# Kernel tuning notes

Measured on AMD Instinct MI355X. Metric: run time of the kernel, lower is better.

Reference implementation:

```python
import jax, jax.numpy as jnp
import numpy as np

# WAGE-style quantizer (NeuroSim training path): round to 2^(b-1) levels, clip to (-1+1/S, 1-1/S),
# straight-through estimator for gradients.

def wage_q(x, bits=8):
    S = 2.0 ** (bits - 1)
    q = jnp.clip(jnp.round(x * S) / S, -1.0 + 1.0 / S, 1.0 - 1.0 / S)
    return x + jax.lax.stop_gradient(q - x)


def qconv(x, w, stride, pad, wl_w=8, wl_a=8):
    wq = wage_q(w, wl_w)
    y = jax.lax.conv_general_dilated(
        x, wq, window_strides=(stride, stride),
        padding=[(pad, pad), (pad, pad)],
        dimension_numbers=('NCHW', 'OIHW', 'NCHW'))
    return wage_q(y, wl_a)


def pad_hw(x, p):
    return jnp.pad(x, ((0, 0), (0, 0), (p, p), (p, p)))


def crop_like(x, tgt):
    return x[:, :, :tgt.shape[2], :tgt.shape[3]]


WEIGHT_SHAPES = {
    'w1': (64, 4, 3, 3), 'w2': (128, 64, 3, 3), 'w3': (256, 128, 3, 3), 'w4': (512, 256, 3, 3),
    'wr11': (512, 512, 3, 3), 'wr12': (512, 512, 3, 3), 'wr21': (512, 512, 3, 3), 'wr22': (512, 512, 3, 3),
    'wd3': (128, 512, 4, 4), 'wd2': (64, 416, 4, 4), 'wd1': (4, 224, 4, 4),
    'wu43': (32, 512, 4, 4), 'wu32': (32, 416, 4, 4), 'wu21': (32, 224, 4, 4), 'wu10': (32, 100, 4, 4),
    'wfc': (1, 32),
}


def setup_inputs() -> dict:
    key = jax.random.key(0)
    keys = jax.random.split(key, len(WEIGHT_SHAPES) + 1)
    inp = {'x': jax.random.normal(keys[0], (8, 4, 256, 256), dtype=jnp.float32)}
    for i, (name, shp) in enumerate(WEIGHT_SHAPES.items()):
        fan_in = int(np.prod(shp[1:]))
        inp[name] = jax.random.normal(keys[i + 1], shp, dtype=jnp.float32) / np.sqrt(fan_in)
    return inp


def reference(x, w1, w2, w3, w4, wr11, wr12, wr21, wr22,
              wd3, wd2, wd1, wu43, wu32, wu21, wu10, wfc):
    c1 = qconv(x, w1, 2, 1)        # [B,64,128,128]
    c2 = qconv(c1, w2, 2, 1)       # [B,128,64,64]
    c3 = qconv(c2, w3, 2, 1)       # [B,256,32,32]
    c4 = qconv(c3, w4, 2, 1)       # [B,512,16,16]
    r11 = qconv(c4, wr11, 1, 1)
    r12 = (1.0 - qconv(r11, wr12, 1, 1)) * c4
    r21 = qconv(r12, wr21, 1, 1)
    r22 = (1.0 - qconv(r21, wr22, 1, 1)) * r12
    r22p = pad_hw(r22, 8)                                   # [B,512,32,32]
    flow4_up = crop_like(qconv(r22p, wu43, 1, 2), c3)       # [B,32,32,32]
    d3 = crop_like(qconv(r22p, wd3, 1, 2), c3)              # [B,128,32,32]
    cat3 = pad_hw(jnp.concatenate([c3, d3, flow4_up], 1), 16)  # [B,416,64,64]
    flow3_up = crop_like(qconv(cat3, wu32, 1, 2), c2)
    d2 = crop_like(qconv(cat3, wd2, 1, 2), c2)
    cat2 = pad_hw(jnp.concatenate([c2, d2, flow3_up], 1), 32)  # [B,224,128,128]
    flow2_up = crop_like(qconv(cat2, wu21, 1, 2), c1)
    d1 = crop_like(qconv(cat2, wd1, 1, 2), c1)
    cat1 = pad_hw(jnp.concatenate([c1, d1, flow2_up], 1), 64)  # [B,100,256,256]
    u10 = qconv(cat1, wu10, 1, 2)                              # [B,32,257,257]
    feat = jnp.max(u10, axis=(2, 3))                           # AdaptiveMaxPool2d((1,1))
    out = wage_q(feat @ wage_q(wfc, 8).T, 8)                   # QLinear 32->1
    return out
```

## Files before the change

### kernel.cpp

```cpp
#include <hip/hip_runtime.h>

#define DEV __device__ __forceinline__

typedef __attribute__((ext_vector_type(4))) int i32x4;

DEV int wqi(float y) {
    int q = (int)rintf(y * 128.0f);
    return q < -127 ? -127 : (q > 127 ? 127 : q);
}
DEV unsigned encf(float f) { unsigned u = __float_as_uint(f); return (u & 0x80000000u) ? ~u : (u | 0x80000000u); }
DEV float decf(unsigned u) { return (u & 0x80000000u) ? __uint_as_float(u ^ 0x80000000u) : __uint_as_float(~u); }
DEV float wq8f(float x) {
    float q = rintf(x * 128.0f) * 0.0078125f;
    return fminf(fmaxf(q, -0.9921875f), 0.9921875f);
}

#define GLOAD16(g, l) __builtin_amdgcn_global_load_lds( \
    (const __attribute__((address_space(1))) void*)(g), \
    (__attribute__((address_space(3))) void*)(l), 16, 0, 0)

struct PackDesc {
    const float* w0; const float* w1; uint4* dst;
    int OC0, OC1, CinW, K, noct, nch64u, ndup, gsz;
};
struct PackArgs { PackDesc d[11]; int bofs[12]; };

__global__ void __launch_bounds__(256) k_packall(PackArgs a) {
    __shared__ unsigned char sb[16 * (64 * 16 + 4)];
    const int b = blockIdx.x;
    int i = 0;
    #pragma unroll
    for (int j = 1; j < 11; ++j) if (b >= a.bofs[j]) i = j;
    const PackDesc D = a.d[i];
    const int b2 = b - a.bofs[i];
    const int oct = b2 % D.noct;
    const int ch64u = b2 / D.noct;
    const int K2 = D.K * D.K;
    const int NCHT = D.nch64u * D.ndup;
    const int row_elems = 64 * K2;
    const int SSTR = row_elems + 4;
    const int QR = row_elems / 4;
    const int NQ = 16 * QR;
    const int cin0 = ch64u * 64;
    const int tid = threadIdx.x;
    const int og = oct / D.gsz, ol = oct % D.gsz;

    for (int q = tid; q < NQ; q += 256) {
        const int r = q / QR, j = q - r * QR;
        const int oc = oct * 16 + r;
        const float* src = nullptr; int oci = 0;
        if (oc < D.OC0) { src = D.w0; oci = oc; }
        else if (oc < D.OC0 + D.OC1) { src = D.w1; oci = oc - D.OC0; }
        const int e0 = j * 4;
        float v[4] = {0.f, 0.f, 0.f, 0.f};
        if (src != nullptr) {
            const float* p = src + ((size_t)oci * D.CinW + cin0) * K2 + e0;
            const int cin_last = cin0 + (e0 + 3) / K2;
            if (cin_last < D.CinW) {
                const float4 f4 = *(const float4*)p;
                v[0] = f4.x; v[1] = f4.y; v[2] = f4.z; v[3] = f4.w;
            } else {
                #pragma unroll
                for (int e = 0; e < 4; ++e) {
                    const int cin = cin0 + (e0 + e) / K2;
                    if (cin < D.CinW) v[e] = p[e];
                }
            }
        }
        unsigned pk = 0;
        #pragma unroll
        for (int e = 0; e < 4; ++e) pk |= ((unsigned)(wqi(v[e]) & 255)) << (e * 8);
        *(unsigned*)&sb[r * SSTR + e0] = pk;
    }
    __syncthreads();

    const int outN = K2 * 64;
    for (int idx = tid; idx < outN; idx += 256) {
        const int kpos = idx >> 6, lane = idx & 63;
        const int l15 = lane & 15, g = lane >> 4;
        unsigned wd[4] = {0u, 0u, 0u, 0u};
        #pragma unroll
        for (int e = 0; e < 16; ++e) {
            const unsigned bval = sb[l15 * SSTR + (g * 16 + e) * K2 + kpos];
            wd[e >> 2] |= bval << ((e & 3) * 8);
        }
        uint4 u; u.x = wd[0]; u.y = wd[1]; u.z = wd[2]; u.w = wd[3];
        for (int d = 0; d < D.ndup; ++d) {
            const int ch64 = ch64u + d * D.nch64u;
            D.dst[((size_t)((og * NCHT + ch64) * K2 + kpos) * D.gsz + ol) * 64 + lane] = u;
        }
    }
}

__global__ void __launch_bounds__(256) k_prep(unsigned* __restrict__ feat, uint4* __restrict__ zbuf,
                                              uint4* __restrict__ ps0,
                                              uint4* __restrict__ z1, uint4* __restrict__ z2,
                                              uint4* __restrict__ z3) {
    int b = blockIdx.x;
    const int tid = threadIdx.x;
    uint4 z; z.x = z.y = z.z = z.w = 0u;
    if (b == 0) {
        feat[tid] = encf(0.0f);
        if (tid < 64) zbuf[tid] = z;
        return;
    }
    b -= 1;
    if (b < 1024) { ps0[b * 256 + tid] = z; return; }
    b -= 1024;
    if (b < 1536) {
        const int i = b * 256 + tid;
        if (i < 393216) { const int pix = i / 3, j = i - pix * 3; z1[(size_t)pix * 7 + 4 + j] = z; }
        return;
    }
    b -= 1536;
    if (b < 768) {
        const int i = b * 256 + tid;
        if (i < 196608) { const int pix = i / 6, j = i - pix * 6; z2[(size_t)pix * 14 + 8 + j] = z; }
        return;
    }
    b -= 768;
    {
        const int i = b * 256 + tid;
        if (i < 81920) { const int pix = i / 10, j = i - pix * 10; z3[(size_t)pix * 26 + 16 + j] = z; }
    }
}

__global__ void __launch_bounds__(256) k_conv1(const float* __restrict__ x, const float* __restrict__ w1,
                                               signed char* __restrict__ cat1) {
    __shared__ float sw2[36][64];
    __shared__ float sin_[4][17][17];
    const int tid = threadIdx.x;
    const int n = blockIdx.y;
    const int oh0 = (blockIdx.x >> 4) * 8, ow0 = (blockIdx.x & 15) * 8;
    for (int i = tid; i < 2304; i += 256) sw2[i % 36][i / 36] = wq8f(w1[i]);
    const int ih0 = oh0 * 2 - 1, iw0 = ow0 * 2 - 1;
    for (int i = tid; i < 4 * 289; i += 256) {
        const int c = i / 289, rem = i % 289, r = rem / 17, cc = rem % 17;
        const int ih = ih0 + r, iw = iw0 + cc;
        float v = 0.f;
        if ((unsigned)ih < 256u && (unsigned)iw < 256u) v = x[((size_t)(n * 4 + c) * 256 + ih) * 256 + iw];
        sin_[c][r][cc] = v;
    }
    __syncthreads();
    const int sp = tid & 63, ocg = tid >> 6;
    const int oh = sp >> 3, ow = sp & 7;
    float acc[16];
    #pragma unroll
    for (int j = 0; j < 16; ++j) acc[j] = 0.f;
    #pragma unroll
    for (int c = 0; c < 4; ++c)
    #pragma unroll
    for (int kh = 0; kh < 3; ++kh)
    #pragma unroll
    for (int kw = 0; kw < 3; ++kw) {
        const float v = sin_[c][oh * 2 + kh][ow * 2 + kw];
        const float4* wp4 = (const float4*)&sw2[c * 9 + kh * 3 + kw][ocg * 16];
        #pragma unroll
        for (int q = 0; q < 4; ++q) {
            const float4 wv = wp4[q];
            acc[q * 4 + 0] = fmaf(v, wv.x, acc[q * 4 + 0]);
            acc[q * 4 + 1] = fmaf(v, wv.y, acc[q * 4 + 1]);
            acc[q * 4 + 2] = fmaf(v, wv.z, acc[q * 4 + 2]);
            acc[q * 4 + 3] = fmaf(v, wv.w, acc[q * 4 + 3]);
        }
    }
    const size_t pix = ((size_t)(n * 128) + oh0 + oh) * 128 + ow0 + ow;
    unsigned wd[4] = {0u, 0u, 0u, 0u};
    #pragma unroll
    for (int j = 0; j < 16; ++j)
        wd[j >> 2] |= ((unsigned)(wqi(acc[j]) & 255)) << ((j & 3) * 8);
    uint4 u; u.x = wd[0]; u.y = wd[1]; u.z = wd[2]; u.w = wd[3];
    *(uint4*)(cat1 + pix * 112 + ocg * 16) = u;
}

__global__ void k_fc(const unsigned* __restrict__ feat, const float* __restrict__ wfc,
                     float* __restrict__ out) {
    int n = threadIdx.x;
    if (n < 8) {
        float s = 0.f;
        for (int c = 0; c < 32; ++c) s += decf(feat[n * 32 + c]) * wq8f(wfc[c]);
        out[n] = wq8f(s);
    }
}

template<int CMODE>
__global__ void __launch_bounds__(256) k_comb(const int* __restrict__ ps, int D, int G,
                                              int NP, int OC, double inv,
                                              signed char* __restrict__ dst, int dstr, int dch,
                                              const void* __restrict__ res, int rstr,
                                              signed char* __restrict__ dhl, int dhlstr,
                                              short* __restrict__ dj,
                                              int ohw, int OWW, int r0, int r1, int c0, int c1,
                                              int* __restrict__ zp) {
    const int t = blockIdx.x * 256 + threadIdx.x;
    const int opc = OC / 4;
    const int total = NP * opc;
    if (t >= total) return;
    const int pix = t / opc, oc0 = (t - pix * opc) * 4;
    const int sp = pix % ohw;
    const int oh = sp / OWW, ow = sp - oh * OWW;
    if (oh < r0 || oh > r1 || ow < c0 || ow > c1) return;
    const size_t base = (size_t)pix * OC + oc0;
    const size_t NPOC = (size_t)NP * OC;
    long v[4] = {0, 0, 0, 0};
    int sidx = 0;
    for (int d = 0; d < D; ++d) {
        long s0 = 0, s1 = 0, s2 = 0, s3 = 0;
        for (int g = 0; g < G; ++g, ++sidx) {
            const int4 p = *(const int4*)(ps + sidx * NPOC + base);
            s0 += p.x; s1 += p.y; s2 += p.z; s3 += p.w;
        }
        v[0] = v[0] * 256 + s0; v[1] = v[1] * 256 + s1;
        v[2] = v[2] * 256 + s2; v[3] = v[3] * 256 + s3;
    }
    if (zp) { int4 z; z.x = z.y = z.z = z.w = 0; *(int4*)(zp + base) = z; }
    if constexpr (CMODE == 0) {
        unsigned pk = 0;
        #pragma unroll
        for (int j = 0; j < 4; ++j)
            pk |= (unsigned)(wqi((float)((double)v[j] * inv)) & 255) << (j * 8);
        *(unsigned*)(dst + (size_t)pix * dstr + dch + oc0) = pk;
    } else {
        #pragma unroll
        for (int j = 0; j < 4; ++j) {
            const int qi = wqi((float)((double)v[j] * inv));
            const int oc = oc0 + j;
            if constexpr (CMODE == 1) {
                const int rv = (int)((const signed char*)res)[(size_t)pix * rstr + oc];
                const int jj = (128 - qi) * rv;
                const int d0 = ((jj + 128) & 255) - 128;
                const int t1 = (jj - d0) >> 8;
                dhl[(size_t)pix * dhlstr + oc] = (signed char)t1;
                dhl[(size_t)pix * dhlstr + 512 + oc] = (signed char)d0;
                dj[(size_t)pix * 512 + oc] = (short)jj;
            } else {
                const int rv = (int)((const short*)res)[(size_t)pix * rstr + oc];
                const int jj = (128 - qi) * rv;
                const int d0 = ((jj + 128) & 255) - 128;
                const int t1 = (jj - d0) >> 8;
                const int d1 = ((t1 + 128) & 255) - 128;
                const int d2 = (t1 - d1) >> 8;
                dhl[(size_t)pix * dhlstr + oc] = (signed char)d2;
                dhl[(size_t)pix * dhlstr + 512 + oc] = (signed char)d1;
                dhl[(size_t)pix * dhlstr + 1024 + oc] = (signed char)d0;
            }
        }
    }
}

template<int K, int STR, int WM, int WN, int BN, int CHQ, int NBUF, int MODE>
__global__ void __launch_bounds__(256) k_mconv(
    const signed char* __restrict__ s0, int Ctot, int st0,
    int S, int padeff,
    const uint4* __restrict__ wqp, int nchtot,
    signed char* __restrict__ dst, int dstr, int dch,
    unsigned* __restrict__ feat, int* __restrict__ ps,
    const signed char* __restrict__ zbuf,
    int OCv, int OH, int OW, int TILES_W, int nch,
    int NT, int NOCG, int swzq, int ORD, int ohb, int owb)
{
    constexpr int TH = WM * 4;
    constexpr int RH = (TH - 1) * STR + K, RW = 7 * STR + K;
    constexpr int UNITS = CHQ / 16;
    constexpr int UPPS = UNITS + 1;
    constexpr int NKC = CHQ / 64;
    constexpr int K2 = K * K;
    constexpr int NUS = RH * RW * UPPS;
    constexpr int ROUNDS = (NUS + 255) / 256;
    constexpr int NUPS = ROUNDS * 256;
    constexpr int AHEAD = NBUF - 1;
    __shared__ uint4 lds[NBUF * NUPS];
    __shared__ int sred[4][2][16];

    const int tid = threadIdx.x, lane = tid & 63, w = tid >> 6;
    const int wm = w % WM, wn = w / WM;
    const int l15 = lane & 15, g = lane >> 4;

    const int b = blockIdx.x;
    const int work = (b & 7) * swzq + (b >> 3);
    int tile, n, ocg, slice;
    if (ORD == 0) {
        ocg = work % NOCG; const int t2 = work / NOCG;
        tile = t2 % NT; const int t3 = t2 / NT;
        n = t3 & 7; slice = t3 >> 3;
    } else {
        tile = work % NT; const int t2 = work / NT;
        n = t2 & 7; const int t3 = t2 >> 3;
        ocg = t3 % NOCG; slice = t3 / NOCG;
    }
    const int cin_off = slice * nch * CHQ;
    const int group = ocg * WN + wn;

    const int tileh = tile / TILES_W, tilew = tile % TILES_W;
    const int oh0 = ohb + tileh * TH, ow0 = owb + tilew * 8;
    const int ih0 = oh0 * STR - padeff, iw0 = ow0 * STR - padeff;
    const int blk_oct0 = ocg * (WN * BN);

    int pixb[2];
    #pragma unroll
    for (int am = 0; am < 2; ++am) {
        const int sp = wm * 32 + am * 16 + l15;
        pixb[am] = ((sp >> 3) * STR) * RW + (sp & 7) * STR;
    }

    int climit[ROUNDS];
    const signed char* gpb[ROUNDS];
    #pragma unroll
    for (int rd = 0; rd < ROUNDS; ++rd) {
        const int d = rd * 256 + tid;
        int cl = -1;
        const signed char* gb = zbuf;
        if (d < NUS) {
            const int pix = d / UPPS;
            const int u = d - pix * UPPS;
            const int r = pix / RW, c = pix - r * RW;
            const int ih = ih0 + r, iw = iw0 + c;
            if (u < UNITS && (unsigned)ih < (unsigned)S && (unsigned)iw < (unsigned)S) {
                cl = Ctot - cin_off - u * 16;
                gb = s0 + (((size_t)n * S + ih) * S + iw) * st0 + cin_off + u * 16;
            }
        }
        climit[rd] = cl; gpb[rd] = gb;
    }

    i32x4 acc[2][BN];
    #pragma unroll
    for (int am = 0; am < 2; ++am)
        #pragma unroll
        for (int bn = 0; bn < BN; ++bn) acc[am][bn] = (i32x4){0, 0, 0, 0};

    auto issue = [&](int ch, int buf) {
        uint4* lb = &lds[buf * NUPS];
        const int chv = ch * CHQ;
        #pragma unroll
        for (int rd = 0; rd < ROUNDS; ++rd) {
            const signed char* gp = (chv < climit[rd]) ? (gpb[rd] + chv) : zbuf;
            GLOAD16(gp, lb + rd * 256 + (tid & ~63));
        }
    };

    #pragma unroll
    for (int i = 0; i < AHEAD; ++i) if (i < nch) issue(i, i % NBUF);

    for (int ch = 0; ch < nch; ++ch) {
        if (ch + AHEAD < nch) issue(ch + AHEAD, (ch + AHEAD) % NBUF);
        const int infl = (nch - 1 - ch < AHEAD) ? nch - 1 - ch : AHEAD;
        if (infl >= 2)      __builtin_amdgcn_s_waitcnt(0xF70 | (2 * ROUNDS));
        else if (infl == 1) __builtin_amdgcn_s_waitcnt(0xF70 | ROUNDS);
        else                __builtin_amdgcn_s_waitcnt(0xF70);
        __builtin_amdgcn_s_barrier();
        __builtin_amdgcn_sched_barrier(0);
        const int bufo = (ch % NBUF) * NUPS;
        const int pb0 = bufo + pixb[0] * UPPS + g;
        const int pb1 = bufo + pixb[1] * UPPS + g;
        const uint4* wrow = wqp + ((size_t)(group * nchtot + (slice * nch + ch) * NKC) * K2 * BN) * 64 + lane;
        #pragma unroll
        for (int kpos = 0; kpos < K2; ++kpos) {
            const int kh = kpos / K, kw = kpos % K;
            const int po = (kh * RW + kw) * UPPS;
            #pragma unroll
            for (int kc = 0; kc < NKC; ++kc) {
                i32x4 bfr[BN];
                #pragma unroll
                for (int bn = 0; bn < BN; ++bn) {
                    union { uint4 u; i32x4 v; } bu;
                    bu.u = wrow[(kc * K2 * BN + kpos * BN + bn) * 64];
                    bfr[bn] = bu.v;
                }
                union { uint4 u; i32x4 v; } a0, a1;
                a0.u = lds[pb0 + po + kc * 4];
                a1.u = lds[pb1 + po + kc * 4];
                #pragma unroll
                for (int bn = 0; bn < BN; ++bn) {
                    acc[0][bn] = __builtin_amdgcn_mfma_i32_16x16x64_i8(a0.v, bfr[bn], acc[0][bn], 0, 0, 0);
                    acc[1][bn] = __builtin_amdgcn_mfma_i32_16x16x64_i8(a1.v, bfr[bn], acc[1][bn], 0, 0, 0);
                }
            }
        }
        __builtin_amdgcn_sched_barrier(0);
        __builtin_amdgcn_s_barrier();
    }

    if constexpr (MODE == 2) {
        #pragma unroll
        for (int bn = 0; bn < BN; ++bn) {
            int m = (int)0x80000000;
            #pragma unroll
            for (int am = 0; am < 2; ++am)
                #pragma unroll
                for (int rg = 0; rg < 4; ++rg) {
                    const int sp = wm * 32 + am * 16 + g * 4 + rg;
                    const int oh = oh0 + (sp >> 3), ow = ow0 + (sp & 7);
                    const int v = acc[am][bn][rg];
                    if (oh < OH && ow < OW && v > m) m = v;
                }
            int o = __shfl_xor(m, 16); if (o > m) m = o;
            o = __shfl_xor(m, 32); if (o > m) m = o;
            if (lane < 16) sred[w][bn][l15] = m;
        }
        __syncthreads();
        if (tid < BN * 16) {
            const int bn = tid >> 4, l = tid & 15;
            int mm = sred[0][bn][l];
            #pragma unroll
            for (int i = 1; i < WM * WN; ++i) { const int o = sred[i][bn][l]; if (o > mm) mm = o; }
            const float y = (float)mm * (1.f / 16384.f);
            const float v = (float)wqi(y) * 0.0078125f;
            atomicMax(&feat[n * 32 + (blk_oct0 + bn) * 16 + l], encf(v));
        }
    } else if constexpr (MODE == 3) {
        #pragma unroll
        for (int am = 0; am < 2; ++am)
        #pragma unroll
        for (int bn = 0; bn < BN; ++bn)
        #pragma unroll
        for (int rg = 0; rg < 4; ++rg) {
            const int sp = wm * 32 + am * 16 + g * 4 + rg;
            const int oh = oh0 + (sp >> 3), ow = ow0 + (sp & 7);
            const int oc = (blk_oct0 + wn * BN + bn) * 16 + l15;
            if (oh < OH && ow < OW && oc < OCv) {
                ps[(((size_t)slice * 8 + n) * OH * OW + (size_t)oh * OW + ow) * OCv + oc] = acc[am][bn][rg];
            }
        }
    } else if constexpr (MODE == 4) {
        #pragma unroll
        for (int am = 0; am < 2; ++am)
        #pragma unroll
        for (int bn = 0; bn < BN; ++bn)
        #pragma unroll
        for (int rg = 0; rg < 4; ++rg) {
            const int sp = wm * 32 + am * 16 + g * 4 + rg;
            const int oh = oh0 + (sp >> 3), ow = ow0 + (sp & 7);
            const int oc = (blk_oct0 + wn * BN + bn) * 16 + l15;
            if (oh < OH && ow < OW && oc < OCv) {
                atomicAdd(&ps[((size_t)n * OH * OW + (size_t)oh * OW + ow) * OCv + oc], acc[am][bn][rg]);
            }
        }
    } else {
        #pragma unroll
        for (int am = 0; am < 2; ++am)
        #pragma unroll
        for (int bn = 0; bn < BN; ++bn)
        #pragma unroll
        for (int rg = 0; rg < 4; ++rg) {
            const int sp = wm * 32 + am * 16 + g * 4 + rg;
            const int oh = oh0 + (sp >> 3), ow = ow0 + (sp & 7);
            const int oc = (blk_oct0 + wn * BN + bn) * 16 + l15;
            if (oh < OH && ow < OW && oc < OCv) {
                const size_t pixo = (size_t)(n * OH + oh) * OW + ow;
                const float y = (float)acc[am][bn][rg] * (1.f / 16384.f);
                dst[pixo * dstr + dch + oc] = (signed char)wqi(y);
            }
        }
    }
}

extern "C" void kernel_launch(void* const* d_in, const int* in_sizes, int n_in,
                              void* d_out, int out_size, void* d_ws, size_t ws_size,
                              hipStream_t stream)
{
    (void)in_sizes; (void)n_in; (void)out_size; (void)ws_size;
    const float* x = (const float*)d_in[0];
    const float* wfc = (const float*)d_in[16];
    float* out = (float*)d_out;

    char* ws = (char*)d_ws;
    size_t off = 0;
    auto alloc = [&](size_t bytes) { char* p = ws + off; off += (bytes + 255) & ~(size_t)255; return p; };

    struct PH { int i0, OC0, i1, OC1, CinW, K, noct, nch64u, ndup, gsz; };
    static const PH ph[11] = {
        {2, 128, -1, 0,  64, 3,  8, 1, 1, 2},
        {3, 256, -1, 0, 128, 3, 16, 2, 1, 2},
        {4, 512, -1, 0, 256, 3, 32, 4, 1, 2},
        {5, 512, -1, 0, 512, 3, 32, 8, 1, 2},
        {6, 512, -1, 0, 512, 3, 32, 8, 1, 2},
        {7, 512, -1, 0, 512, 3, 32, 8, 2, 2},
        {8, 512, -1, 0, 512, 3, 32, 8, 1, 2},
        {9, 128, 12, 32, 512, 4, 12, 8, 3, 2},
        {10, 64, 13, 32, 416, 4,  6, 7, 1, 2},
        {11,  4, 14, 32, 224, 4,  3, 4, 1, 3},
        {15, 32, -1, 0, 100, 4,  2, 2, 1, 2}};

    PackArgs pa;
    int bacc = 0;
    uint4* wp[11];
    for (int i = 0; i < 11; ++i) {
        const int nch64 = ph[i].nch64u * ph[i].ndup;
        const int nel = nch64 * ph[i].K * ph[i].K * ph[i].noct * 64;
        wp[i] = (uint4*)alloc((size_t)nel * 16);
        pa.d[i].w0 = (const float*)d_in[ph[i].i0];
        pa.d[i].w1 = (ph[i].i1 >= 0) ? (const float*)d_in[ph[i].i1] : nullptr;
        pa.d[i].dst = wp[i];
        pa.d[i].OC0 = ph[i].OC0; pa.d[i].OC1 = ph[i].OC1;
        pa.d[i].CinW = ph[i].CinW; pa.d[i].K = ph[i].K; pa.d[i].noct = ph[i].noct;
        pa.d[i].nch64u = ph[i].nch64u; pa.d[i].ndup = ph[i].ndup;
        pa.d[i].gsz = ph[i].gsz;
        pa.bofs[i] = bacc;
        bacc += ph[i].noct * ph[i].nch64u;
    }
    pa.bofs[11] = bacc;

    signed char* cat1b = (signed char*)alloc((size_t)8*128*128*112);
    signed char* cat2b = (signed char*)alloc((size_t)8*64*64*224);
    signed char* cat3b = (signed char*)alloc((size_t)8*32*32*416);
    signed char* c4b   = (signed char*)alloc((size_t)8*16*16*512);
    signed char* r11b  = (signed char*)alloc((size_t)8*16*16*512);
    signed char* r12d  = (signed char*)alloc((size_t)8*16*16*1024);
    short*       r12j  = (short*)alloc((size_t)8*16*16*512 * 2);
    signed char* r22d  = (signed char*)alloc((size_t)8*16*16*1536);
    int*         psum  = (int*)alloc((size_t)6*8*32*32*160 * 4);
    unsigned*    featb = (unsigned*)alloc(256 * 4);
    uint4*       zbuf  = (uint4*)alloc(1024);

    k_packall<<<dim3((unsigned)bacc), dim3(256), 0, stream>>>(pa);
    k_prep<<<dim3(3649), 256, 0, stream>>>(featb, zbuf, (uint4*)psum,
        (uint4*)cat1b, (uint4*)cat2b, (uint4*)cat3b);
    k_conv1<<<dim3(256, 8), dim3(256), 0, stream>>>(x, (const float*)d_in[1], cat1b);

    const signed char* zb = (const signed char*)zbuf;
    const void* nv = nullptr;
    const int BIG = 1 << 30;

    k_mconv<3,2,2,2,2,64,1,0><<<dim3(1024), 256, 0, stream>>>(
        cat1b,64,112, 128,1, wp[0],1, cat2b,224,0, nullptr,nullptr, zb,
        128,64,64,8, 1, 64,2,128, 0, 0,0);
    k_mconv<3,2,2,2,2,64,2,0><<<dim3(512), 256, 0, stream>>>(
        cat2b,128,224, 64,1, wp[1],2, cat3b,416,0, nullptr,nullptr, zb,
        256,32,32,4, 2, 16,4,64, 0, 0,0);
    k_mconv<3,2,2,2,2,64,1,4><<<dim3(1024), 256, 0, stream>>>(
        cat3b,256,416, 32,1, wp[2],4, nullptr,0,0, nullptr,(int*)psum, zb,
        512,16,16,2, 1, 4,8,128, 1, 0,0);
    k_comb<0><<<dim3(1024), 256, 0, stream>>>(psum,1,1, 2048,512, 1.0/16384.0, c4b,512,0, nv,0, nullptr,0,nullptr,
        256,16, 0,BIG,0,BIG, psum);
    k_mconv<3,1,2,2,2,128,1,4><<<dim3(1024), 256, 0, stream>>>(
        c4b,512,512, 16,1, wp[3],8, nullptr,0,0, nullptr,psum, zb,
        512,16,16,2, 1, 4,8,128, 1, 0,0);
    k_comb<0><<<dim3(1024), 256, 0, stream>>>(psum,1,1, 2048,512, 1.0/16384.0, r11b,512,0, nv,0, nullptr,0,nullptr,
        256,16, 0,BIG,0,BIG, psum);
    k_mconv<3,1,2,2,2,128,1,4><<<dim3(512), 256, 0, stream>>>(
        r11b,512,512, 16,1, wp[4],8, nullptr,0,0, nullptr,psum, zb,
        512,16,16,2, 2, 4,8,64, 1, 0,0);
    k_comb<1><<<dim3(1024), 256, 0, stream>>>(psum,1,1, 2048,512, 1.0/16384.0, nullptr,0,0, c4b,512, r12d,1024,r12j,
        256,16, 0,BIG,0,BIG, nullptr);
    k_mconv<3,1,2,2,2,128,1,3><<<dim3(1024), 256, 0, stream>>>(
        r12d,1024,1024, 16,1, wp[5],16, nullptr,0,0, nullptr,psum, zb,
        512,16,16,2, 2, 4,8,128, 1, 0,0);
    k_comb<0><<<dim3(1024), 256, 0, stream>>>(psum,2,2, 2048,512, 1.0/2097152.0, r11b,512,0, nv,0, nullptr,0,nullptr,
        256,16, 0,BIG,0,BIG, psum);
    k_mconv<3,1,2,2,2,128,1,4><<<dim3(512), 256, 0, stream>>>(
        r11b,512,512, 16,1, wp[6],8, nullptr,0,0, nullptr,psum, zb,
        512,16,16,2, 2, 4,8,64, 1, 0,0);
    k_comb<2><<<dim3(1024), 256, 0, stream>>>(psum,1,1, 2048,512, 1.0/16384.0, nullptr,0,0, r12j,512, r22d,1536,nullptr,
        256,16, 0,BIG,0,BIG, nullptr);
    k_mconv<4,1,2,2,2,128,1,3><<<dim3(648), 256, 0, stream>>>(
        r22d,1536,1536, 16,10, wp[7],24, nullptr,0,0, nullptr,psum, zb,
        160,32,32,3, 4, 9,3,81, 1, 7,7);
    k_comb<0><<<dim3(1280), 256, 0, stream>>>(psum,3,1, 8192,160, 1.0/268435456.0, cat3b,416,256, nv,0, nullptr,0,nullptr,
        1024,32, 7,25,7,25, nullptr);
    k_mconv<4,1,4,1,2,64,2,0><<<dim3(360), 256, 0, stream>>>(
        cat3b,416,416, 32,18, wp[8],7, cat2b,224,128, nullptr,nullptr, zb,
        96,64,64,5, 7, 15,3,45, 0, 15,15);
    k_mconv<4,1,4,1,3,64,2,0><<<dim3(360), 256, 0, stream>>>(
        cat2b,224,224, 64,34, wp[9],4, cat1b,112,64, nullptr,nullptr, zb,
        48,128,128,9, 4, 45,1,45, 0, 31,31);
    k_mconv<4,1,4,1,2,128,1,2><<<dim3(1224), 256, 0, stream>>>(
        cat1b,112,112, 128,66, wp[10],2, nullptr,0,0, featb,nullptr, zb,
        32,257,257,17, 1, 153,1,153, 0, 63,63);
    k_fc<<<dim3(1), dim3(64), 0, stream>>>(featb, wfc, out);
}
```

Baseline: 294.7 us.

## Parameterize MFMA row-tiles per warp and retile 16x16 layers for weight reuse

Adds an AM template parameter so each warp can compute a variable number of 16-pixel row tiles, then retiles the 16x16 residual/bottleneck convolutions to WM=1, WN=4, AM=4. Each weight fragment loaded from global is now reused across four A tiles instead of two, and warps split output channels instead of pixels. Split-K slice counts, chunk sizes and grid sizes change to match, along with the psum buffer size and the k_comb reduction counts. This raises accumulator register pressure and changes LDS tile shapes and parallelism per layer.

```diff
diff --git a/kernel.cpp b/kernel.cpp
--- a/kernel.cpp
+++ b/kernel.cpp
@@ -248,7 +248,7 @@
     }
 }
 
-template<int K, int STR, int WM, int WN, int BN, int CHQ, int NBUF, int MODE>
+template<int K, int STR, int WM, int WN, int BN, int AM, int CHQ, int NBUF, int MODE>
 __global__ void __launch_bounds__(256) k_mconv(
     const signed char* __restrict__ s0, int Ctot, int st0,
     int S, int padeff,
@@ -259,7 +259,7 @@
     int OCv, int OH, int OW, int TILES_W, int nch,
     int NT, int NOCG, int swzq, int ORD, int ohb, int owb)
 {
-    constexpr int TH = WM * 4;
+    constexpr int TH = WM * AM * 2;
     constexpr int RH = (TH - 1) * STR + K, RW = 7 * STR + K;
     constexpr int UNITS = CHQ / 16;
     constexpr int UPPS = UNITS + 1;
@@ -296,10 +296,10 @@
     const int ih0 = oh0 * STR - padeff, iw0 = ow0 * STR - padeff;
     const int blk_oct0 = ocg * (WN * BN);
 
-    int pixb[2];
-    #pragma unroll
-    for (int am = 0; am < 2; ++am) {
-        const int sp = wm * 32 + am * 16 + l15;
+    int pixb[AM];
+    #pragma unroll
+    for (int am = 0; am < AM; ++am) {
+        const int sp = (wm * AM + am) * 16 + l15;
         pixb[am] = ((sp >> 3) * STR) * RW + (sp & 7) * STR;
     }
 
@@ -323,9 +323,9 @@
         climit[rd] = cl; gpb[rd] = gb;
     }
 
-    i32x4 acc[2][BN];
-    #pragma unroll
-    for (int am = 0; am < 2; ++am)
+    i32x4 acc[AM][BN];
+    #pragma unroll
+    for (int am = 0; am < AM; ++am)
         #pragma unroll
         for (int bn = 0; bn < BN; ++bn) acc[am][bn] = (i32x4){0, 0, 0, 0};
 
@@ -351,8 +351,9 @@
         __builtin_amdgcn_s_barrier();
         __builtin_amdgcn_sched_barrier(0);
         const int bufo = (ch % NBUF) * NUPS;
-        const int pb0 = bufo + pixb[0] * UPPS + g;
-        const int pb1 = bufo + pixb[1] * UPPS + g;
+        int pbs[AM];
+        #pragma unroll
+        for (int am = 0; am < AM; ++am) pbs[am] = bufo + pixb[am] * UPPS + g;
         const uint4* wrow = wqp + ((size_t)(group * nchtot + (slice * nch + ch) * NKC) * K2 * BN) * 64 + lane;
         #pragma unroll
         for (int kpos = 0; kpos < K2; ++kpos) {
@@ -367,13 +368,13 @@
                     bu.u = wrow[(kc * K2 * BN + kpos * BN + bn) * 64];
                     bfr[bn] = bu.v;
                 }
-                union { uint4 u; i32x4 v; } a0, a1;
-                a0.u = lds[pb0 + po + kc * 4];
-                a1.u = lds[pb1 + po + kc * 4];
                 #pragma unroll
-                for (int bn = 0; bn < BN; ++bn) {
-                    acc[0][bn] = __builtin_amdgcn_mfma_i32_16x16x64_i8(a0.v, bfr[bn], acc[0][bn], 0, 0, 0);
-                    acc[1][bn] = __builtin_amdgcn_mfma_i32_16x16x64_i8(a1.v, bfr[bn], acc[1][bn], 0, 0, 0);
+                for (int am = 0; am < AM; ++am) {
+                    union { uint4 u; i32x4 v; } a0;
+                    a0.u = lds[pbs[am] + po + kc * 4];
+                    #pragma unroll
+                    for (int bn = 0; bn < BN; ++bn)
+                        acc[am][bn] = __builtin_amdgcn_mfma_i32_16x16x64_i8(a0.v, bfr[bn], acc[am][bn], 0, 0, 0);
                 }
             }
         }
@@ -386,10 +387,10 @@
         for (int bn = 0; bn < BN; ++bn) {
             int m = (int)0x80000000;
             #pragma unroll
-            for (int am = 0; am < 2; ++am)
+            for (int am = 0; am < AM; ++am)
                 #pragma unroll
                 for (int rg = 0; rg < 4; ++rg) {
-                    const int sp = wm * 32 + am * 16 + g * 4 + rg;
+                    const int sp = (wm * AM + am) * 16 + g * 4 + rg;
                     const int oh = oh0 + (sp >> 3), ow = ow0 + (sp & 7);
                     const int v = acc[am][bn][rg];
                     if (oh < OH && ow < OW && v > m) m = v;
@@ -410,12 +411,12 @@
         }
     } else if constexpr (MODE == 3) {
         #pragma unroll
-        for (int am = 0; am < 2; ++am)
+        for (int am = 0; am < AM; ++am)
         #pragma unroll
         for (int bn = 0; bn < BN; ++bn)
         #pragma unroll
         for (int rg = 0; rg < 4; ++rg) {
-            const int sp = wm * 32 + am * 16 + g * 4 + rg;
+            const int sp = (wm * AM + am) * 16 + g * 4 + rg;
             const int oh = oh0 + (sp >> 3), ow = ow0 + (sp & 7);
             const int oc = (blk_oct0 + wn * BN + bn) * 16 + l15;
             if (oh < OH && ow < OW && oc < OCv) {
@@ -424,12 +425,12 @@
         }
     } else if constexpr (MODE == 4) {
         #pragma unroll
-        for (int am = 0; am < 2; ++am)
+        for (int am = 0; am < AM; ++am)
         #pragma unroll
         for (int bn = 0; bn < BN; ++bn)
         #pragma unroll
         for (int rg = 0; rg < 4; ++rg) {
-            const int sp = wm * 32 + am * 16 + g * 4 + rg;
+            const int sp = (wm * AM + am) * 16 + g * 4 + rg;
             const int oh = oh0 + (sp >> 3), ow = ow0 + (sp & 7);
             const int oc = (blk_oct0 + wn * BN + bn) * 16 + l15;
             if (oh < OH && ow < OW && oc < OCv) {
@@ -438,12 +439,12 @@
         }
     } else {
         #pragma unroll
-        for (int am = 0; am < 2; ++am)
+        for (int am = 0; am < AM; ++am)
         #pragma unroll
         for (int bn = 0; bn < BN; ++bn)
         #pragma unroll
         for (int rg = 0; rg < 4; ++rg) {
-            const int sp = wm * 32 + am * 16 + g * 4 + rg;
+            const int sp = (wm * AM + am) * 16 + g * 4 + rg;
             const int oh = oh0 + (sp >> 3), ow = ow0 + (sp & 7);
             const int oc = (blk_oct0 + wn * BN + bn) * 16 + l15;
             if (oh < OH && ow < OW && oc < OCv) {
@@ -477,7 +478,7 @@
         {6, 512, -1, 0, 512, 3, 32, 8, 1, 2},
         {7, 512, -1, 0, 512, 3, 32, 8, 2, 2},
         {8, 512, -1, 0, 512, 3, 32, 8, 1, 2},
-        {9, 128, 12, 32, 512, 4, 12, 8, 3, 2},
+        {9, 128, 12, 32, 512, 4, 16, 8, 3, 2},
         {10, 64, 13, 32, 416, 4,  6, 7, 1, 2},
         {11,  4, 14, 32, 224, 4,  3, 4, 1, 3},
         {15, 32, -1, 0, 100, 4,  2, 2, 1, 2}};
@@ -509,7 +510,7 @@
     signed char* r12d  = (signed char*)alloc((size_t)8*16*16*1024);
     short*       r12j  = (short*)alloc((size_t)8*16*16*512 * 2);
     signed char* r22d  = (signed char*)alloc((size_t)8*16*16*1536);
-    int*         psum  = (int*)alloc((size_t)6*8*32*32*160 * 4);
+    int*         psum  = (int*)alloc((size_t)8*8*16*16*512 * 4);
     unsigned*    featb = (unsigned*)alloc(256 * 4);
     uint4*       zbuf  = (uint4*)alloc(1024);
 
@@ -522,49 +523,49 @@
     const void* nv = nullptr;
     const int BIG = 1 << 30;
 
-    k_mconv<3,2,2,2,2,64,1,0><<<dim3(1024), 256, 0, stream>>>(
+    k_mconv<3,2,2,2,2,2,64,1,0><<<dim3(1024), 256, 0, stream>>>(
         cat1b,64,112, 128,1, wp[0],1, cat2b,224,0, nullptr,nullptr, zb,
         128,64,64,8, 1, 64,2,128, 0, 0,0);
-    k_mconv<3,2,2,2,2,64,2,0><<<dim3(512), 256, 0, stream>>>(
+    k_mconv<3,2,2,2,2,2,64,2,0><<<dim3(512), 256, 0, stream>>>(
         cat2b,128,224, 64,1, wp[1],2, cat3b,416,0, nullptr,nullptr, zb,
         256,32,32,4, 2, 16,4,64, 0, 0,0);
-    k_mconv<3,2,2,2,2,64,1,4><<<dim3(1024), 256, 0, stream>>>(
+    k_mconv<3,2,1,4,2,4,64,1,4><<<dim3(512), 256, 0, stream>>>(
         cat3b,256,416, 32,1, wp[2],4, nullptr,0,0, nullptr,(int*)psum, zb,
-        512,16,16,2, 1, 4,8,128, 1, 0,0);
+        512,16,16,2, 1, 4,4,64, 1, 0,0);
     k_comb<0><<<dim3(1024), 256, 0, stream>>>(psum,1,1, 2048,512, 1.0/16384.0, c4b,512,0, nv,0, nullptr,0,nullptr,
         256,16, 0,BIG,0,BIG, psum);
-    k_mconv<3,1,2,2,2,128,1,4><<<dim3(1024), 256, 0, stream>>>(
+    k_mconv<3,1,1,4,2,4,64,1,4><<<dim3(1024), 256, 0, stream>>>(
         c4b,512,512, 16,1, wp[3],8, nullptr,0,0, nullptr,psum, zb,
-        512,16,16,2, 1, 4,8,128, 1, 0,0);
+        512,16,16,2, 1, 4,4,128, 1, 0,0);
     k_comb<0><<<dim3(1024), 256, 0, stream>>>(psum,1,1, 2048,512, 1.0/16384.0, r11b,512,0, nv,0, nullptr,0,nullptr,
         256,16, 0,BIG,0,BIG, psum);
-    k_mconv<3,1,2,2,2,128,1,4><<<dim3(512), 256, 0, stream>>>(
+    k_mconv<3,1,1,4,2,4,64,1,4><<<dim3(1024), 256, 0, stream>>>(
         r11b,512,512, 16,1, wp[4],8, nullptr,0,0, nullptr,psum, zb,
-        512,16,16,2, 2, 4,8,64, 1, 0,0);
+        512,16,16,2, 1, 4,4,128, 1, 0,0);
     k_comb<1><<<dim3(1024), 256, 0, stream>>>(psum,1,1, 2048,512, 1.0/16384.0, nullptr,0,0, c4b,512, r12d,1024,r12j,
         256,16, 0,BIG,0,BIG, nullptr);
-    k_mconv<3,1,2,2,2,128,1,3><<<dim3(1024), 256, 0, stream>>>(
+    k_mconv<3,1,1,4,2,4,128,1,3><<<dim3(1024), 256, 0, stream>>>(
         r12d,1024,1024, 16,1, wp[5],16, nullptr,0,0, nullptr,psum, zb,
-        512,16,16,2, 2, 4,8,128, 1, 0,0);
-    k_comb<0><<<dim3(1024), 256, 0, stream>>>(psum,2,2, 2048,512, 1.0/2097152.0, r11b,512,0, nv,0, nullptr,0,nullptr,
+        512,16,16,2, 1, 4,4,128, 1, 0,0);
+    k_comb<0><<<dim3(1024), 256, 0, stream>>>(psum,2,4, 2048,512, 1.0/2097152.0, r11b,512,0, nv,0, nullptr,0,nullptr,
         256,16, 0,BIG,0,BIG, psum);
-    k_mconv<3,1,2,2,2,128,1,4><<<dim3(512), 256, 0, stream>>>(
+    k_mconv<3,1,1,4,2,4,64,1,4><<<dim3(1024), 256, 0, stream>>>(
         r11b,512,512, 16,1, wp[6],8, nullptr,0,0, nullptr,psum, zb,
-        512,16,16,2, 2, 4,8,64, 1, 0,0);
+        512,16,16,2, 1, 4,4,128, 1, 0,0);
     k_comb<2><<<dim3(1024), 256, 0, stream>>>(psum,1,1, 2048,512, 1.0/16384.0, nullptr,0,0, r12j,512, r22d,1536,nullptr,
         256,16, 0,BIG,0,BIG, nullptr);
-    k_mconv<4,1,2,2,2,128,1,3><<<dim3(648), 256, 0, stream>>>(
+    k_mconv<4,1,1,4,2,4,128,1,3><<<dim3(864), 256, 0, stream>>>(
         r22d,1536,1536, 16,10, wp[7],24, nullptr,0,0, nullptr,psum, zb,
-        160,32,32,3, 4, 9,3,81, 1, 7,7);
-    k_comb<0><<<dim3(1280), 256, 0, stream>>>(psum,3,1, 8192,160, 1.0/268435456.0, cat3b,416,256, nv,0, nullptr,0,nullptr,
+        160,32,32,3, 2, 9,2,108, 1, 7,7);
+    k_comb<0><<<dim3(1280), 256, 0, stream>>>(psum,3,2, 8192,160, 1.0/268435456.0, cat3b,416,256, nv,0, nullptr,0,nullptr,
         1024,32, 7,25,7,25, nullptr);
-    k_mconv<4,1,4,1,2,64,2,0><<<dim3(360), 256, 0, stream>>>(
+    k_mconv<4,1,4,1,2,2,64,2,0><<<dim3(360), 256, 0, stream>>>(
         cat3b,416,416, 32,18, wp[8],7, cat2b,224,128, nullptr,nullptr, zb,
         96,64,64,5, 7, 15,3,45, 0, 15,15);
-    k_mconv<4,1,4,1,3,64,2,0><<<dim3(360), 256, 0, stream>>>(
+    k_mconv<4,1,4,1,3,2,64,2,0><<<dim3(360), 256, 0, stream>>>(
         cat2b,224,224, 64,34, wp[9],4, cat1b,112,64, nullptr,nullptr, zb,
         48,128,128,9, 4, 45,1,45, 0, 31,31);
-    k_mconv<4,1,4,1,2,128,1,2><<<dim3(1224), 256, 0, stream>>>(
+    k_mconv<4,1,4,1,2,2,128,1,2><<<dim3(1224), 256, 0, stream>>>(
         cat1b,112,112, 128,66, wp[10],2, nullptr,0,0, featb,nullptr, zb,
         32,257,257,17, 1, 153,1,153, 0, 63,63);
     k_fc<<<dim3(1), dim3(64), 0, stream>>>(featb, wfc, out);
```

Measured after the change: 320.5 us. +8.8%, slower.
